# Kernel tuning notes

Measured on AMD Instinct MI355X. Metric: run time of the kernel, lower is better.

## Reference

```python
import jax, jax.numpy as jnp
import numpy as np
import math

HEADS = 8
DIM_HEAD = 64
NUM_BUCKETS = 32
MAX_DISTANCE = 128


def _relative_position_bucket(relative_position, num_buckets=NUM_BUCKETS, max_distance=MAX_DISTANCE):
    # T5-style bucketing, faithful to RelativePositionBias._relative_position_bucket
    n = -relative_position
    num_buckets = num_buckets // 2
    ret = (n < 0).astype(jnp.int32) * num_buckets
    n = jnp.abs(n)
    max_exact = num_buckets // 2
    is_small = n < max_exact
    # guard log(0); those lanes are masked out by is_small
    val_if_large = max_exact + (
        jnp.log(jnp.maximum(n, 1).astype(jnp.float32) / max_exact)
        / math.log(max_distance / max_exact)
        * (num_buckets - max_exact)
    ).astype(jnp.int32)
    val_if_large = jnp.minimum(val_if_large, num_buckets - 1)
    return ret + jnp.where(is_small, n, val_if_large)


def _time_rel_pos_bias(n_frames, table):
    pos = jnp.arange(n_frames, dtype=jnp.int32)
    rel_pos = pos[None, :] - pos[:, None]           # [f, f] = k_pos - q_pos
    buckets = _relative_position_bucket(rel_pos)    # [f, f] int
    values = table[buckets]                         # [f, f, heads]
    return jnp.transpose(values, (2, 0, 1))         # [heads, f, f]


def setup_inputs() -> dict:
    key = jax.random.key(0)
    ks = jax.random.split(key, 7)
    B, F, C = 8192, 16, 512
    s = 1.0 / math.sqrt(C)
    return {
        "hidden_states": jax.random.normal(ks[0], (B, F, C), jnp.float32),
        "Wq": jax.random.normal(ks[1], (C, C), jnp.float32) * s,
        "Wk": jax.random.normal(ks[2], (C, C), jnp.float32) * s,
        "Wv": jax.random.normal(ks[3], (C, C), jnp.float32) * s,
        "Wo": jax.random.normal(ks[4], (C, C), jnp.float32) * s,
        "bo": jnp.zeros((C,), jnp.float32),
        "rel_bias_table": jax.random.normal(ks[5], (NUM_BUCKETS, HEADS), jnp.float32) * 0.02,
    }


def reference(hidden_states, Wq, Wk, Wv, Wo, bo, rel_bias_table):
    # hidden_states: [B, F, C] where B = batch*spatial, F = n_frames
    b, f, c = hidden_states.shape
    scale = DIM_HEAD ** -0.5

    q = hidden_states @ Wq  # [B, F, C]
    k = hidden_states @ Wk
    v = hidden_states @ Wv

    def split_heads(t):  # [B, F, C] -> [B, H, F, Dh]
        return t.reshape(b, f, HEADS, DIM_HEAD).transpose(0, 2, 1, 3)

    q, k, v = split_heads(q), split_heads(k), split_heads(v)

    bias = _time_rel_pos_bias(f, rel_bias_table)  # [H, F, F]
    scores = jnp.einsum('bhid,bhjd->bhij', q, k) * scale + bias[None]
    probs = jax.nn.softmax(scores, axis=-1)
    out = jnp.einsum('bhij,bhjd->bhid', probs, v)  # [B, H, F, Dh]
    out = out.transpose(0, 2, 1, 3).reshape(b, f, HEADS * DIM_HEAD)
    return out @ Wo + bo
```

## Files before the change

### kernel.cpp

```cpp
#include <hip/hip_runtime.h>
#include <stdint.h>

typedef unsigned short u16;
typedef __attribute__((ext_vector_type(8))) __bf16 bf16x8;
typedef __attribute__((ext_vector_type(4))) float f32x4;

#define GLOBAL_AS __attribute__((address_space(1)))
#define LDS_AS __attribute__((address_space(3)))

__device__ __forceinline__ float bf2f(u16 v) {
  union { uint32_t u; float f; } x; x.u = (uint32_t)v << 16; return x.f;
}
__device__ __forceinline__ u16 f2bf(float f) {
  union { float f; uint32_t u; } x; x.f = f;
  uint32_t u = x.u + 0x7fffu + ((x.u >> 16) & 1u);
  return (u16)(u >> 16);
}

__global__ void pack_weights(const float* __restrict__ Wq, const float* __restrict__ Wk,
                             const float* __restrict__ Wv, const float* __restrict__ Wo,
                             u16* __restrict__ WT) {
  int g = blockIdx.x * 256 + threadIdx.x;
  int n = g >> 9;
  int k = g & 511;
  const float* src = (n < 1024) ? ((n < 512) ? Wq : Wk) : ((n < 1536) ? Wv : Wo);
  WT[g] = f2bf(src[k * 512 + (n & 511)]);
}

__global__ __launch_bounds__(256) void convert_bf16(const float* __restrict__ src,
                                                    u16* __restrict__ dst) {
  long i = ((long)blockIdx.x * 256 + threadIdx.x) * 8;
  float4 a = *(const float4*)(src + i);
  float4 b = *(const float4*)(src + i + 4);
  uint4 w;
  w.x = (uint32_t)f2bf(a.x) | ((uint32_t)f2bf(a.y) << 16);
  w.y = (uint32_t)f2bf(a.z) | ((uint32_t)f2bf(a.w) << 16);
  w.z = (uint32_t)f2bf(b.x) | ((uint32_t)f2bf(b.y) << 16);
  w.w = (uint32_t)f2bf(b.z) | ((uint32_t)f2bf(b.w) << 16);
  *(uint4*)(dst + i) = w;
}

template <bool AF32, bool CF32>
__global__ __launch_bounds__(256, 2) void gemm_core(
    const void* __restrict__ Ap, int lda,
    const u16* __restrict__ BT,
    const float* __restrict__ bias,
    void* __restrict__ Cp, int ldc)
{
  __shared__ __align__(16) u16 lsA[128 * 32];
  __shared__ __align__(16) u16 lsB[128 * 32];

  const int tid  = threadIdx.x;
  const int wave = tid >> 6;
  const int lane = tid & 63;
  const int quad = lane >> 4;
  const int lrow = lane & 15;
  const int wm = wave & 1;
  const int wn = wave >> 1;

  const int gx = gridDim.x;
  int bid = blockIdx.y * gx + blockIdx.x;
  int nwg = gx * gridDim.y;
  int lb = (nwg & 7) ? bid : ((bid & 7) * (nwg >> 3) + (bid >> 3));
  const int  n0 = (lb % gx) * 128;
  const long m0 = (long)(lb / gx) * 128;

  const int s0 = tid, s1 = 256 + tid;
  const u16* bgp0 = BT + (long)(n0 + (s0 >> 2)) * 512 + (s0 & 3) * 8;
  const u16* bgp1 = BT + (long)(n0 + (s1 >> 2)) * 512 + (s1 & 3) * 8;
  u16* lB0 = lsB + wave * 512;
  u16* lB1 = lsB + 2048 + wave * 512;

  const float* agf0 = (const float*)Ap + (m0 + (s0 >> 2)) * (long)lda + (s0 & 3) * 8;
  const float* agf1 = (const float*)Ap + (m0 + (s1 >> 2)) * (long)lda + (s1 & 3) * 8;
  const u16*   agb0 = (const u16*)Ap + (m0 + (s0 >> 2)) * (long)lda + (s0 & 3) * 8;
  const u16*   agb1 = (const u16*)Ap + (m0 + (s1 >> 2)) * (long)lda + (s1 & 3) * 8;
  u16* lA0 = lsA + wave * 512;
  u16* lA1 = lsA + 2048 + wave * 512;

  f32x4 acc[4][4] = {};

  for (int k0 = 0; k0 < 512; k0 += 32) {
    __syncthreads();
    if constexpr (AF32) {
      float4 x0 = *(const float4*)(agf0 + k0);
      float4 x1 = *(const float4*)(agf0 + k0 + 4);
      float4 y0 = *(const float4*)(agf1 + k0);
      float4 y1 = *(const float4*)(agf1 + k0 + 4);
      uint4 w0, w1;
      w0.x = (uint32_t)f2bf(x0.x) | ((uint32_t)f2bf(x0.y) << 16);
      w0.y = (uint32_t)f2bf(x0.z) | ((uint32_t)f2bf(x0.w) << 16);
      w0.z = (uint32_t)f2bf(x1.x) | ((uint32_t)f2bf(x1.y) << 16);
      w0.w = (uint32_t)f2bf(x1.z) | ((uint32_t)f2bf(x1.w) << 16);
      w1.x = (uint32_t)f2bf(y0.x) | ((uint32_t)f2bf(y0.y) << 16);
      w1.y = (uint32_t)f2bf(y0.z) | ((uint32_t)f2bf(y0.w) << 16);
      w1.z = (uint32_t)f2bf(y1.x) | ((uint32_t)f2bf(y1.y) << 16);
      w1.w = (uint32_t)f2bf(y1.z) | ((uint32_t)f2bf(y1.w) << 16);
      *(uint4*)(lsA + s0 * 8) = w0;
      *(uint4*)(lsA + s1 * 8) = w1;
    } else {
      __builtin_amdgcn_global_load_lds((GLOBAL_AS const uint32_t*)(agb0 + k0),
                                       (LDS_AS uint32_t*)lA0, 16, 0, 0);
      __builtin_amdgcn_global_load_lds((GLOBAL_AS const uint32_t*)(agb1 + k0),
                                       (LDS_AS uint32_t*)lA1, 16, 0, 0);
    }
    __builtin_amdgcn_global_load_lds((GLOBAL_AS const uint32_t*)(bgp0 + k0),
                                     (LDS_AS uint32_t*)lB0, 16, 0, 0);
    __builtin_amdgcn_global_load_lds((GLOBAL_AS const uint32_t*)(bgp1 + k0),
                                     (LDS_AS uint32_t*)lB1, 16, 0, 0);
    __syncthreads();

    bf16x8 af[4], bfr[4];
#pragma unroll
    for (int t = 0; t < 4; ++t) {
      af[t]  = *(const bf16x8*)(lsA + (wm * 64 + t * 16 + lrow) * 32 + quad * 8);
      bfr[t] = *(const bf16x8*)(lsB + (wn * 64 + t * 16 + lrow) * 32 + quad * 8);
    }
#pragma unroll
    for (int mt = 0; mt < 4; ++mt)
#pragma unroll
      for (int nt = 0; nt < 4; ++nt)
        acc[mt][nt] = __builtin_amdgcn_mfma_f32_16x16x32_bf16(af[mt], bfr[nt],
                                                              acc[mt][nt], 0, 0, 0);
  }

#pragma unroll
  for (int mt = 0; mt < 4; ++mt) {
    long rbase = m0 + wm * 64 + mt * 16 + quad * 4;
#pragma unroll
    for (int nt = 0; nt < 4; ++nt) {
      int colg = n0 + wn * 64 + nt * 16 + lrow;
      float badd = bias ? bias[colg] : 0.0f;
      f32x4 v = acc[mt][nt];
#pragma unroll
      for (int r = 0; r < 4; ++r) {
        if constexpr (CF32)
          ((float*)Cp)[(rbase + r) * (long)ldc + colg] = v[r] + badd;
        else
          ((u16*)Cp)[(rbase + r) * (long)ldc + colg] = f2bf(v[r] + badd);
      }
    }
  }
}

#define RS 1544

__global__ __launch_bounds__(256) void attn_k(
    u16* __restrict__ qkv, const float* __restrict__ table )
{
  __shared__ __align__(16) u16 sQ[16 * RS];
  __shared__ float S[8 * 16 * 16];
  const int tid = threadIdx.x;
  const long base = (long)blockIdx.x * (16 * 1536);

  {
    const uint4* src = (const uint4*)(qkv + base);
    uint4* dst = (uint4*)sQ;
#pragma unroll
    for (int r = 0; r < 12; ++r) {
      int idx = r * 256 + tid;
      int row = idx / 192;
      int c   = idx - row * 192;
      dst[row * 193 + c] = src[idx];
    }
  }
  __syncthreads();

  {
    const int h = tid >> 5;
    const int slot = tid & 31;
    const int j = slot & 15;
    const int ibase = (slot >> 4) * 8;
    float kr[64];
    const uint4* kp = (const uint4*)(sQ + j * RS + 512 + h * 64);
#pragma unroll
    for (int t = 0; t < 8; ++t) {
      uint4 u = kp[t];
      kr[t * 8 + 0] = bf2f((u16)u.x); kr[t * 8 + 1] = bf2f((u16)(u.x >> 16));
      kr[t * 8 + 2] = bf2f((u16)u.y); kr[t * 8 + 3] = bf2f((u16)(u.y >> 16));
      kr[t * 8 + 4] = bf2f((u16)u.z); kr[t * 8 + 5] = bf2f((u16)(u.z >> 16));
      kr[t * 8 + 6] = bf2f((u16)u.w); kr[t * 8 + 7] = bf2f((u16)(u.w >> 16));
    }
#pragma unroll
    for (int r = 0; r < 8; ++r) {
      int i = ibase + r;
      const uint4* qp = (const uint4*)(sQ + i * RS + h * 64);
      float acc = 0.f;
#pragma unroll
      for (int t = 0; t < 8; ++t) {
        uint4 u = qp[t];
        acc = fmaf(bf2f((u16)u.x),         kr[t * 8 + 0], acc);
        acc = fmaf(bf2f((u16)(u.x >> 16)), kr[t * 8 + 1], acc);
        acc = fmaf(bf2f((u16)u.y),         kr[t * 8 + 2], acc);
        acc = fmaf(bf2f((u16)(u.y >> 16)), kr[t * 8 + 3], acc);
        acc = fmaf(bf2f((u16)u.z),         kr[t * 8 + 4], acc);
        acc = fmaf(bf2f((u16)(u.z >> 16)), kr[t * 8 + 5], acc);
        acc = fmaf(bf2f((u16)u.w),         kr[t * 8 + 6], acc);
        acc = fmaf(bf2f((u16)(u.w >> 16)), kr[t * 8 + 7], acc);
      }
      int n = i - j;
      int an = n < 0 ? -n : n;
      int bb = an < 8 ? an : (an < 12 ? 8 : 9);
      int bucket = (n < 0 ? 16 : 0) + bb;
      S[(h * 16 + i) * 16 + j] = acc * 0.125f + table[bucket * 8 + h];
    }
  }
  __syncthreads();

  if (tid < 128) {
    float* row = S + tid * 16;
    float m = row[0];
#pragma unroll
    for (int j = 1; j < 16; ++j) m = fmaxf(m, row[j]);
    float e[16]; float s = 0.f;
#pragma unroll
    for (int j = 0; j < 16; ++j) { e[j] = __expf(row[j] - m); s += e[j]; }
    float inv = 1.0f / s;
#pragma unroll
    for (int j = 0; j < 16; ++j) row[j] = e[j] * inv;
  }
  __syncthreads();

  {
    const int c8 = tid & 63;
    const int f4 = tid >> 6;
    const int h = c8 >> 3;
    uint4 vv[16];
#pragma unroll
    for (int jj = 0; jj < 16; ++jj)
      vv[jj] = *(const uint4*)(sQ + jj * RS + 1024 + c8 * 8);
#pragma unroll
    for (int ff = 0; ff < 4; ++ff) {
      int f = f4 * 4 + ff;
      const f32x4* p = (const f32x4*)(S + (h * 16 + f) * 16);
      f32x4 p0 = p[0], p1 = p[1], p2 = p[2], p3 = p[3];
      float acc[8] = {};
#pragma unroll
      for (int jj = 0; jj < 16; ++jj) {
        float pj = (jj < 4) ? p0[jj & 3] : (jj < 8) ? p1[jj & 3]
                 : (jj < 12) ? p2[jj & 3] : p3[jj & 3];
        uint4 u = vv[jj];
        acc[0] = fmaf(pj, bf2f((u16)u.x),         acc[0]);
        acc[1] = fmaf(pj, bf2f((u16)(u.x >> 16)), acc[1]);
        acc[2] = fmaf(pj, bf2f((u16)u.y),         acc[2]);
        acc[3] = fmaf(pj, bf2f((u16)(u.y >> 16)), acc[3]);
        acc[4] = fmaf(pj, bf2f((u16)u.z),         acc[4]);
        acc[5] = fmaf(pj, bf2f((u16)(u.z >> 16)), acc[5]);
        acc[6] = fmaf(pj, bf2f((u16)u.w),         acc[6]);
        acc[7] = fmaf(pj, bf2f((u16)(u.w >> 16)), acc[7]);
      }
      uint4 w;
      w.x = (uint32_t)f2bf(acc[0]) | ((uint32_t)f2bf(acc[1]) << 16);
      w.y = (uint32_t)f2bf(acc[2]) | ((uint32_t)f2bf(acc[3]) << 16);
      w.z = (uint32_t)f2bf(acc[4]) | ((uint32_t)f2bf(acc[5]) << 16);
      w.w = (uint32_t)f2bf(acc[6]) | ((uint32_t)f2bf(acc[7]) << 16);
      *(uint4*)(qkv + base + f * 1536 + c8 * 8) = w;
    }
  }
}

extern "C" void kernel_launch(void* const* d_in, const int* in_sizes, int n_in,
                              void* d_out, int out_size, void* d_ws, size_t ws_size,
                              hipStream_t stream) {
  (void)in_sizes; (void)n_in; (void)out_size; (void)ws_size;
  const float* hs = (const float*)d_in[0];
  const float* Wq = (const float*)d_in[1];
  const float* Wk = (const float*)d_in[2];
  const float* Wv = (const float*)d_in[3];
  const float* Wo = (const float*)d_in[4];
  const float* bo = (const float*)d_in[5];
  const float* tb = (const float*)d_in[6];
  float* out = (float*)d_out;

  u16* WT  = (u16*)d_ws;
  u16* qkv = (u16*)((char*)d_ws + (4ull << 20));
  u16* Abf = (u16*)d_out;

  convert_bf16<<<32768, 256, 0, stream>>>(hs, Abf);
  pack_weights<<<4096, 256, 0, stream>>>(Wq, Wk, Wv, Wo, WT);

  dim3 g1(12, 1024);
  gemm_core<false, false><<<g1, 256, 0, stream>>>(Abf, 512, WT, nullptr, qkv, 1536);

  attn_k<<<8192, 256, 0, stream>>>(qkv, tb);

  dim3 g3(4, 1024);
  gemm_core<false, true><<<g3, 256, 0, stream>>>(qkv, 1536, WT + 1536 * 512, bo, out, 512);
}
```

Before: 1.007 ms.

## Fuse output projection into attention kernel using MFMA on LDS-resident result

The attention kernel now writes its per-block output into shared memory instead of back to the global qkv buffer, then multiplies it by Wo with bf16 MFMA instructions and adds the bias, writing fp32 output directly. This removes the separate output GEMM launch and the global round trip of the attention output. In exchange, each of 8192 blocks rereads the whole 512x512 Wo from global memory or cache with no LDS staging, and the output stores are strided per lane.

```diff
diff --git a/kernel.cpp b/kernel.cpp
--- a/kernel.cpp
+++ b/kernel.cpp
@@ -145,8 +145,10 @@
 
 #define RS 1544
 
-__global__ __launch_bounds__(256) void attn_k(
-    u16* __restrict__ qkv, const float* __restrict__ table )
+__global__ __launch_bounds__(256) void attn_proj(
+    const u16* __restrict__ qkv, const u16* __restrict__ WT,
+    const float* __restrict__ bo, const float* __restrict__ table,
+    float* __restrict__ out)
 {
   __shared__ __align__(16) u16 sQ[16 * RS];
   __shared__ float S[8 * 16 * 16];
@@ -254,7 +256,37 @@
       w.y = (uint32_t)f2bf(acc[2]) | ((uint32_t)f2bf(acc[3]) << 16);
       w.z = (uint32_t)f2bf(acc[4]) | ((uint32_t)f2bf(acc[5]) << 16);
       w.w = (uint32_t)f2bf(acc[6]) | ((uint32_t)f2bf(acc[7]) << 16);
-      *(uint4*)(qkv + base + f * 1536 + c8 * 8) = w;
+      *(uint4*)(sQ + f * RS + c8 * 8) = w;
+    }
+  }
+  __syncthreads();
+
+  {
+    const int wave = tid >> 6;
+    const int lane = tid & 63;
+    const int quad = lane >> 4;
+    const int lrow = lane & 15;
+    const u16* WoT = WT + 1536 * 512;
+
+    f32x4 acc[8] = {};
+#pragma unroll
+    for (int k0 = 0; k0 < 512; k0 += 32) {
+      bf16x8 af = *(const bf16x8*)(sQ + lrow * RS + k0 + quad * 8);
+#pragma unroll
+      for (int t = 0; t < 8; ++t) {
+        bf16x8 bf = *(const bf16x8*)(WoT + (wave * 128 + t * 16 + lrow) * 512
+                                     + k0 + quad * 8);
+        acc[t] = __builtin_amdgcn_mfma_f32_16x16x32_bf16(af, bf, acc[t], 0, 0, 0);
+      }
+    }
+    float* op = out + (long)blockIdx.x * 16 * 512;
+#pragma unroll
+    for (int t = 0; t < 8; ++t) {
+      int colg = wave * 128 + t * 16 + lrow;
+      float badd = bo[colg];
+#pragma unroll
+      for (int r = 0; r < 4; ++r)
+        op[(quad * 4 + r) * 512 + colg] = acc[t][r] + badd;
     }
   }
 }
@@ -282,8 +314,5 @@
   dim3 g1(12, 1024);
   gemm_core<false, false><<<g1, 256, 0, stream>>>(Abf, 512, WT, nullptr, qkv, 1536);
 
-  attn_k<<<8192, 256, 0, stream>>>(qkv, tb);
-
-  dim3 g3(4, 1024);
-  gemm_core<false, true><<<g3, 256, 0, stream>>>(qkv, 1536, WT + 1536 * 512, bo, out, 512);
-}
+  attn_proj<<<8192, 256, 0, stream>>>(qkv, WT, bo, tb, out);
+}
```

New measurement: 1.279 ms. 27.0% more time.
